# Kernel tuning notes

Measured on AMD Instinct MI355X. Metric: run time of the kernel, lower is better.

## Reference

```python
import jax, jax.numpy as jnp
import numpy as np

DIM = 1024

def setup_inputs() -> dict:
    key = jax.random.key(0)
    k1, k2, k3, k4 = jax.random.split(key, 4)
    scale = 1.0 / np.sqrt(DIM)
    return {
        "segment_embeds": jax.random.normal(k1, (32, 2048, DIM), dtype=jnp.float32),
        "Wq": jax.random.normal(k2, (DIM, DIM), dtype=jnp.float32) * scale,
        "bq": jax.random.normal(k3, (DIM,), dtype=jnp.float32) * scale,
        "mem_bank": jax.random.normal(k4, (131072, DIM), dtype=jnp.float32) * scale,
        "k": 8,
    }

def reference(segment_embeds, Wq, bq, mem_bank, k):
    # mean-pool over time: (B, C)
    segment_mean = segment_embeds.mean(axis=1)
    # linear query projection (torch Linear: x @ W.T + b)
    q = segment_mean @ Wq.T + bq
    # dense scores against memory bank: (B, M)
    attn_scores = (q @ mem_bank.T) / jnp.sqrt(jnp.asarray(DIM, dtype=q.dtype))
    # top-k select
    top_k_scores, top_k_indices = jax.lax.top_k(attn_scores, k)  # (B, K)
    attn_weights = jax.nn.softmax(top_k_scores, axis=-1)  # (B, K)
    # gather retrieved vectors: (B, K, C)
    retrieved_vectors = mem_bank[top_k_indices]
    # weighted sum over K, keepdim -> (B, 1, C)
    retrieved_mem = jnp.sum(attn_weights[..., None] * retrieved_vectors, axis=1, keepdims=True)
    return retrieved_mem
```

## Files before the change

kernel.cpp:

```cpp
#include <hip/hip_runtime.h>
#include <hip/hip_bf16.h>
#include <math.h>

#define NB 32
#define NT 2048
#define NC 1024
#define NM 131072
#define TOPK 8
#define PANELS 8
#define NSB 1024
#define SLOTF 260

typedef __attribute__((ext_vector_type(8))) short s16x8;
typedef __attribute__((ext_vector_type(4))) float f32x4;
typedef __attribute__((ext_vector_type(4))) int i32x4;

#define OFF_PART 0
#define OFF_CS   0
#define OFF_CI   262144
#define OFF_MEAN 1048576
#define OFF_Q    (OFF_MEAN + 32768)
#define OFF_QB   (OFF_Q + 32768)

__device__ __forceinline__ unsigned short f2bf(float f) {
    unsigned u = __float_as_uint(f);
    unsigned r = (u + 0x7FFFu + ((u >> 16) & 1u)) >> 16;
    return (unsigned short)r;
}

__device__ __forceinline__ void gl_lds16(const float* g, float* l) {
    __builtin_amdgcn_global_load_lds((const __attribute__((address_space(1))) void*)g,
                                     (__attribute__((address_space(3))) void*)l, 16, 0, 0);
}

__global__ __launch_bounds__(256) void mean_partial_k(const float* __restrict__ seg,
                                                      float* __restrict__ part) {
    int blk = blockIdx.x;
    int b = blk >> 5, tc = blk & 31;
    int tid = threadIdx.x;
    const float4* src = (const float4*)(seg + ((size_t)b * NT + (size_t)tc * 64) * NC);
    float4 acc = make_float4(0.f, 0.f, 0.f, 0.f);
#pragma unroll 4
    for (int t = 0; t < 64; ++t) {
        float4 v = src[(size_t)t * 256 + tid];
        acc.x += v.x; acc.y += v.y; acc.z += v.z; acc.w += v.w;
    }
    ((float4*)(part + ((size_t)b * 32 + tc) * NC))[tid] = acc;
}

__global__ __launch_bounds__(256) void mean_finalize_k(const float* __restrict__ part,
                                                       float* __restrict__ mean) {
    int i = blockIdx.x * 256 + threadIdx.x;
    int b = i >> 10, c = i & 1023;
    float s = 0.f;
#pragma unroll
    for (int tc = 0; tc < 32; ++tc) s += part[((size_t)b * 32 + tc) * NC + c];
    mean[i] = s * (1.0f / NT);
}

__global__ __launch_bounds__(256) void qproj_k(const float* __restrict__ mean,
                                               const float* __restrict__ Wq,
                                               const float* __restrict__ bq,
                                               float* __restrict__ q) {
    int wave = (blockIdx.x * 256 + threadIdx.x) >> 6;
    int lane = threadIdx.x & 63;
    int o0 = wave * 16;
    for (int j = 0; j < 16; ++j) {
        int o = o0 + j;
        int b = o >> 10, i = o & 1023;
        const float4* wr = (const float4*)(Wq + (size_t)i * NC);
        const float4* mr = (const float4*)(mean + (size_t)b * NC);
        float acc = 0.f;
#pragma unroll
        for (int e = 0; e < 4; ++e) {
            float4 w4 = wr[lane * 4 + e];
            float4 m4 = mr[lane * 4 + e];
            acc += w4.x * m4.x + w4.y * m4.y + w4.z * m4.z + w4.w * m4.w;
        }
#pragma unroll
        for (int off = 32; off; off >>= 1) acc += __shfl_xor(acc, off);
        if (lane == 0) q[o] = acc + bq[i];
    }
}

__global__ __launch_bounds__(256) void qbf_k(const float* __restrict__ q,
                                             s16x8* __restrict__ qb) {
    int idx = blockIdx.x * 256 + threadIdx.x;
    int lane = idx & 63, n = (idx >> 6) & 1, ks = idx >> 7;
    int b = n * 16 + (lane & 15);
    int k0 = ks * 32 + ((lane >> 4) << 3);
    s16x8 v;
#pragma unroll
    for (int e = 0; e < 8; ++e) v[e] = (short)f2bf(q[(size_t)b * NC + k0 + e]);
    qb[idx] = v;
}

#define BUBBLE8(v, vi, s, si)                                   \
    {                                                           \
        float _v = (v); int _vi = (vi);                         \
        _Pragma("unroll")                                       \
        for (int _u = 0; _u < 8; ++_u) {                        \
            bool _gt = _v > s[_u];                               \
            float _ts = _gt ? _v : s[_u];                       \
            int _ti = _gt ? _vi : si[_u];                       \
            _v = _gt ? s[_u] : _v;                              \
            _vi = _gt ? si[_u] : _vi;                           \
            s[_u] = _ts; si[_u] = _ti;                          \
        }                                                       \
    }

__global__ __launch_bounds__(64) void scores_mfma_k(const float* __restrict__ memb,
                                                    const s16x8* __restrict__ qb,
                                                    float* __restrict__ candS,
                                                    int* __restrict__ candI) {
    __shared__ __align__(16) float tiles[2 * 16 * SLOTF];
    __shared__ __align__(16) float sc[32 * 17];
    int lane = threadIdx.x;
    size_t mb0 = (size_t)blockIdx.x * (PANELS * 16);

    float s8[8]; int i8[8];
#pragma unroll
    for (int u = 0; u < 8; ++u) { s8[u] = -INFINITY; i8[u] = -1; }

#define TISSUE(t_) { int p_ = (t_) >> 2, c_ = (t_) & 3;                               \
    const float* rb_ = memb + (mb0 + p_ * 16) * NC + c_ * 256 + lane * 4;             \
    float* lb_ = tiles + ((t_) & 1) * (16 * SLOTF);                                   \
    _Pragma("unroll") for (int i_ = 0; i_ < 16; ++i_)                                 \
        gl_lds16(rb_ + (size_t)i_ * NC, lb_ + i_ * SLOTF); }

    f32x4 acc0 = (f32x4){0.f, 0.f, 0.f, 0.f};
    f32x4 acc1 = (f32x4){0.f, 0.f, 0.f, 0.f};

    TISSUE(0);
    for (int t = 0; t < PANELS * 4; ++t) {
        int c = t & 3;
        s16x8 qf[16];
#pragma unroll
        for (int k = 0; k < 8; ++k) {
            qf[2 * k]     = qb[((c * 8 + k) * 2 + 0) * 64 + lane];
            qf[2 * k + 1] = qb[((c * 8 + k) * 2 + 1) * 64 + lane];
        }
        asm volatile("s_waitcnt vmcnt(0)" ::: "memory");
        __builtin_amdgcn_sched_barrier(0);
        if (t + 1 < PANELS * 4) TISSUE(t + 1);

        const float* lanebase = tiles + (t & 1) * (16 * SLOTF)
                              + (lane & 15) * SLOTF + ((lane >> 4) << 3);
#pragma unroll
        for (int ks = 0; ks < 8; ++ks) {
            uint4 lo = *(const uint4*)(lanebase + ks * 32);
            uint4 hi = *(const uint4*)(lanebase + ks * 32 + 4);
            i32x4 ai;
            ai[0] = __builtin_amdgcn_perm(lo.y, lo.x, 0x07060302u);
            ai[1] = __builtin_amdgcn_perm(lo.w, lo.z, 0x07060302u);
            ai[2] = __builtin_amdgcn_perm(hi.y, hi.x, 0x07060302u);
            ai[3] = __builtin_amdgcn_perm(hi.w, hi.z, 0x07060302u);
            s16x8 a = __builtin_bit_cast(s16x8, ai);
            acc0 = __builtin_amdgcn_mfma_f32_16x16x32_bf16(a, qf[2 * ks], acc0, 0, 0, 0);
            acc1 = __builtin_amdgcn_mfma_f32_16x16x32_bf16(a, qf[2 * ks + 1], acc1, 0, 0, 0);
        }

        if (c == 3) {
            int p = t >> 2;
#pragma unroll
            for (int j = 0; j < 4; ++j) {
                sc[(0 * 16 + (lane & 15)) * 17 + ((lane >> 4) << 2) + j] = acc0[j];
                sc[(1 * 16 + (lane & 15)) * 17 + ((lane >> 4) << 2) + j] = acc1[j];
            }
            asm volatile("s_waitcnt lgkmcnt(0)" ::: "memory");
            __builtin_amdgcn_sched_barrier(0);
            int b = lane >> 1, p2 = lane & 1;
            int midx0 = mb0 + p * 16;
#pragma unroll
            for (int j = 0; j < 8; ++j) {
                int m = ((b + j) & 7) + p2 * 8;
                float v = sc[b * 17 + m];
                BUBBLE8(v, midx0 + m, s8, i8);
            }
            asm volatile("s_waitcnt lgkmcnt(0)" ::: "memory");
            __builtin_amdgcn_sched_barrier(0);
            acc0 = (f32x4){0.f, 0.f, 0.f, 0.f};
            acc1 = (f32x4){0.f, 0.f, 0.f, 0.f};
        }
    }
#undef TISSUE

    {
        float ov[8]; int oi[8];
#pragma unroll
        for (int u = 0; u < 8; ++u) { ov[u] = s8[u]; oi[u] = i8[u]; }
#pragma unroll
        for (int u = 0; u < 8; ++u) {
            float pv = __shfl_xor(ov[u], 1);
            int pi = __shfl_xor(oi[u], 1);
            BUBBLE8(pv, pi, s8, i8);
        }
        if ((lane & 1) == 0) {
            int b = lane >> 1;
#pragma unroll
            for (int u = 0; u < 8; ++u) {
                candS[(size_t)b * (NSB * 8) + blockIdx.x * 8 + u] = s8[u] * 0.03125f;
                candI[(size_t)b * (NSB * 8) + blockIdx.x * 8 + u] = i8[u];
            }
        }
    }
}

__global__ __launch_bounds__(256) void finalize_k(const float* __restrict__ candS,
                                                  const int* __restrict__ candI,
                                                  const float* __restrict__ memb,
                                                  const float* __restrict__ q,
                                                  float* __restrict__ out) {
    __shared__ float cs[256 * 9];
    __shared__ int ci[256 * 9];
    __shared__ float csA[64 * 9];
    __shared__ int ciA[64 * 9];
    __shared__ float exsc[64];
    __shared__ int exid[64];
    __shared__ float wgt[8];
    __shared__ int widx[8];
    int b = blockIdx.x, tid = threadIdx.x;
    const float* S = candS + (size_t)b * (NSB * 8);
    const int* I = candI + (size_t)b * (NSB * 8);

    {
        float s[8]; int si[8];
#pragma unroll
        for (int u = 0; u < 8; ++u) { s[u] = -INFINITY; si[u] = -1; }
        for (int j = 0; j < 32; ++j)
            BUBBLE8(S[tid * 32 + j], I[tid * 32 + j], s, si);
#pragma unroll
        for (int u = 0; u < 8; ++u) { cs[tid * 9 + u] = s[u]; ci[tid * 9 + u] = si[u]; }
    }
    __syncthreads();
    if (tid < 64) {
        float s[8]; int si[8];
#pragma unroll
        for (int u = 0; u < 8; ++u) { s[u] = -INFINITY; si[u] = -1; }
        for (int tt = 0; tt < 4; ++tt)
#pragma unroll
            for (int u = 0; u < 8; ++u)
                BUBBLE8(cs[(tid * 4 + tt) * 9 + u], ci[(tid * 4 + tt) * 9 + u], s, si);
#pragma unroll
        for (int u = 0; u < 8; ++u) { csA[tid * 9 + u] = s[u]; ciA[tid * 9 + u] = si[u]; }
    }
    __syncthreads();
    if (tid < 8) {
        float s[8]; int si[8];
#pragma unroll
        for (int u = 0; u < 8; ++u) { s[u] = -INFINITY; si[u] = -1; }
        for (int tt = 0; tt < 8; ++tt)
#pragma unroll
            for (int u = 0; u < 8; ++u)
                BUBBLE8(csA[(tid * 8 + tt) * 9 + u], ciA[(tid * 8 + tt) * 9 + u], s, si);
#pragma unroll
        for (int u = 0; u < 8; ++u) exid[tid * 8 + u] = si[u];
    }
    __syncthreads();
    {
        int w = tid >> 6, lane = tid & 63;
        const float4* qr = (const float4*)(q + (size_t)b * NC);
        for (int i = 0; i < 16; ++i) {
            int c = w * 16 + i;
            int row = exid[c];
            const float4* mr = (const float4*)(memb + (size_t)row * NC);
            float d = 0.f;
#pragma unroll
            for (int e = 0; e < 4; ++e) {
                float4 m4 = mr[e * 64 + lane];
                float4 q4 = qr[e * 64 + lane];
                d += m4.x * q4.x + m4.y * q4.y + m4.z * q4.z + m4.w * q4.w;
            }
#pragma unroll
            for (int off = 32; off; off >>= 1) d += __shfl_xor(d, off);
            if (lane == 0) exsc[c] = d * 0.03125f;
        }
    }
    __syncthreads();
    if (tid == 0) {
        float s4[8]; int si4[8];
#pragma unroll
        for (int u = 0; u < 8; ++u) { s4[u] = -INFINITY; si4[u] = -1; }
        for (int j = 0; j < 64; ++j)
            BUBBLE8(exsc[j], exid[j], s4, si4);
        float m = s4[0], sum = 0.f, w[8];
#pragma unroll
        for (int u = 0; u < 8; ++u) { w[u] = __expf(s4[u] - m); sum += w[u]; }
        float inv = 1.0f / sum;
#pragma unroll
        for (int u = 0; u < 8; ++u) { wgt[u] = w[u] * inv; widx[u] = si4[u]; }
    }
    __syncthreads();
    {
        float wv[8]; int ix[8];
#pragma unroll
        for (int u = 0; u < 8; ++u) { wv[u] = wgt[u]; ix[u] = widx[u]; }
        float4 o = make_float4(0.f, 0.f, 0.f, 0.f);
#pragma unroll
        for (int u = 0; u < 8; ++u) {
            float4 r = ((const float4*)(memb + (size_t)ix[u] * NC))[tid];
            o.x = fmaf(wv[u], r.x, o.x);
            o.y = fmaf(wv[u], r.y, o.y);
            o.z = fmaf(wv[u], r.z, o.z);
            o.w = fmaf(wv[u], r.w, o.w);
        }
        ((float4*)(out + (size_t)b * NC))[tid] = o;
    }
}

extern "C" void kernel_launch(void* const* d_in, const int* in_sizes, int n_in,
                              void* d_out, int out_size, void* d_ws, size_t ws_size,
                              hipStream_t stream) {
    const float* seg  = (const float*)d_in[0];
    const float* Wq   = (const float*)d_in[1];
    const float* bq   = (const float*)d_in[2];
    const float* memb = (const float*)d_in[3];
    float* ws = (float*)d_ws;
    float* part  = ws + OFF_PART;
    float* mean  = ws + OFF_MEAN;
    float* q     = ws + OFF_Q;
    s16x8* qb    = (s16x8*)(ws + OFF_QB);
    float* candS = ws + OFF_CS;
    int*   candI = (int*)(ws + OFF_CI);
    float* out = (float*)d_out;

    mean_partial_k<<<NB * 32, 256, 0, stream>>>(seg, part);
    mean_finalize_k<<<(NB * NC) / 256, 256, 0, stream>>>(part, mean);
    qproj_k<<<512, 256, 0, stream>>>(mean, Wq, bq, q);
    qbf_k<<<16, 256, 0, stream>>>(q, qb);
    scores_mfma_k<<<NSB, 64, 0, stream>>>(memb, qb, candS, candI);
    finalize_k<<<NB, 256, 0, stream>>>(candS, candI, memb, q, out);
}
```

Measured before the change: 213.6 us.

## Triple-buffer memory-bank tiles with deeper prefetch and double-buffered query fragments

```diff
diff --git a/kernel.cpp b/kernel.cpp
--- a/kernel.cpp
+++ b/kernel.cpp
@@ -7,8 +7,9 @@
 #define NC 1024
 #define NM 131072
 #define TOPK 8
-#define PANELS 8
-#define NSB 1024
+#define PANELS 16
+#define NSB 512
+#define NCHUNK (PANELS * 4)
 #define SLOTF 260
 
 typedef __attribute__((ext_vector_type(8))) short s16x8;
@@ -17,7 +18,7 @@
 
 #define OFF_PART 0
 #define OFF_CS   0
-#define OFF_CI   262144
+#define OFF_CI   131072
 #define OFF_MEAN 1048576
 #define OFF_Q    (OFF_MEAN + 32768)
 #define OFF_QB   (OFF_Q + 32768)
@@ -109,11 +110,11 @@
         }                                                       \
     }
 
-__global__ __launch_bounds__(64) void scores_mfma_k(const float* __restrict__ memb,
-                                                    const s16x8* __restrict__ qb,
-                                                    float* __restrict__ candS,
-                                                    int* __restrict__ candI) {
-    __shared__ __align__(16) float tiles[2 * 16 * SLOTF];
+__global__ __launch_bounds__(64, 1) void scores_mfma_k(const float* __restrict__ memb,
+                                                       const s16x8* __restrict__ qb,
+                                                       float* __restrict__ candS,
+                                                       int* __restrict__ candI) {
+    __shared__ __align__(16) float tiles[3 * 16 * SLOTF];
     __shared__ __align__(16) float sc[32 * 17];
     int lane = threadIdx.x;
     size_t mb0 = (size_t)blockIdx.x * (PANELS * 16);
@@ -124,66 +125,85 @@
 
 #define TISSUE(t_) { int p_ = (t_) >> 2, c_ = (t_) & 3;                               \
     const float* rb_ = memb + (mb0 + p_ * 16) * NC + c_ * 256 + lane * 4;             \
-    float* lb_ = tiles + ((t_) & 1) * (16 * SLOTF);                                   \
+    float* lb_ = tiles + ((t_) % 3) * (16 * SLOTF);                                   \
     _Pragma("unroll") for (int i_ = 0; i_ < 16; ++i_)                                 \
         gl_lds16(rb_ + (size_t)i_ * NC, lb_ + i_ * SLOTF); }
 
+#define QLOAD(dst_, t_) { int c_ = (t_) & 3;                                          \
+    _Pragma("unroll") for (int k_ = 0; k_ < 8; ++k_) {                                \
+        dst_[2 * k_]     = qb[((c_ * 8 + k_) * 2 + 0) * 64 + lane];                   \
+        dst_[2 * k_ + 1] = qb[((c_ * 8 + k_) * 2 + 1) * 64 + lane]; } }
+
+#define COMPUTE(t_, qf_) {                                                            \
+    const float* lanebase = tiles + ((t_) % 3) * (16 * SLOTF)                         \
+                          + (lane & 15) * SLOTF + ((lane >> 4) << 3);                 \
+    _Pragma("unroll") for (int ks = 0; ks < 8; ++ks) {                                \
+        uint4 lo = *(const uint4*)(lanebase + ks * 32);                               \
+        uint4 hi = *(const uint4*)(lanebase + ks * 32 + 4);                           \
+        i32x4 ai;                                                                     \
+        ai[0] = __builtin_amdgcn_perm(lo.y, lo.x, 0x07060302u);                       \
+        ai[1] = __builtin_amdgcn_perm(lo.w, lo.z, 0x07060302u);                       \
+        ai[2] = __builtin_amdgcn_perm(hi.y, hi.x, 0x07060302u);                       \
+        ai[3] = __builtin_amdgcn_perm(hi.w, hi.z, 0x07060302u);                       \
+        s16x8 a = __builtin_bit_cast(s16x8, ai);                                      \
+        acc0 = __builtin_amdgcn_mfma_f32_16x16x32_bf16(a, qf_[2 * ks], acc0, 0, 0, 0);\
+        acc1 = __builtin_amdgcn_mfma_f32_16x16x32_bf16(a, qf_[2 * ks + 1], acc1, 0, 0, 0); } \
+    if (((t_) & 3) == 3) {                                                            \
+        int p_ = (t_) >> 2;                                                           \
+        _Pragma("unroll") for (int j = 0; j < 4; ++j) {                               \
+            sc[(0 * 16 + (lane & 15)) * 17 + ((lane >> 4) << 2) + j] = acc0[j];       \
+            sc[(1 * 16 + (lane & 15)) * 17 + ((lane >> 4) << 2) + j] = acc1[j];       \
+        }                                                                             \
+        asm volatile("s_waitcnt lgkmcnt(0)" ::: "memory");                            \
+        __builtin_amdgcn_sched_barrier(0);                                            \
+        int b_ = lane >> 1, p2_ = lane & 1;                                           \
+        int midx0 = (int)mb0 + p_ * 16;                                               \
+        _Pragma("unroll") for (int j = 0; j < 8; ++j) {                               \
+            int m_ = ((b_ + j) & 7) + p2_ * 8;                                        \
+            float v_ = sc[b_ * 17 + m_];                                              \
+            BUBBLE8(v_, midx0 + m_, s8, i8);                                          \
+        }                                                                             \
+        asm volatile("s_waitcnt lgkmcnt(0)" ::: "memory");                            \
+        __builtin_amdgcn_sched_barrier(0);                                            \
+        acc0 = (f32x4){0.f, 0.f, 0.f, 0.f};                                           \
+        acc1 = (f32x4){0.f, 0.f, 0.f, 0.f};                                           \
+    } }
+
     f32x4 acc0 = (f32x4){0.f, 0.f, 0.f, 0.f};
     f32x4 acc1 = (f32x4){0.f, 0.f, 0.f, 0.f};
+    s16x8 qfA[16], qfB[16];
 
     TISSUE(0);
-    for (int t = 0; t < PANELS * 4; ++t) {
-        int c = t & 3;
-        s16x8 qf[16];
-#pragma unroll
-        for (int k = 0; k < 8; ++k) {
-            qf[2 * k]     = qb[((c * 8 + k) * 2 + 0) * 64 + lane];
-            qf[2 * k + 1] = qb[((c * 8 + k) * 2 + 1) * 64 + lane];
-        }
-        asm volatile("s_waitcnt vmcnt(0)" ::: "memory");
-        __builtin_amdgcn_sched_barrier(0);
-        if (t + 1 < PANELS * 4) TISSUE(t + 1);
-
-        const float* lanebase = tiles + (t & 1) * (16 * SLOTF)
-                              + (lane & 15) * SLOTF + ((lane >> 4) << 3);
-#pragma unroll
-        for (int ks = 0; ks < 8; ++ks) {
-            uint4 lo = *(const uint4*)(lanebase + ks * 32);
-            uint4 hi = *(const uint4*)(lanebase + ks * 32 + 4);
-            i32x4 ai;
-            ai[0] = __builtin_amdgcn_perm(lo.y, lo.x, 0x07060302u);
-            ai[1] = __builtin_amdgcn_perm(lo.w, lo.z, 0x07060302u);
-            ai[2] = __builtin_amdgcn_perm(hi.y, hi.x, 0x07060302u);
-            ai[3] = __builtin_amdgcn_perm(hi.w, hi.z, 0x07060302u);
-            s16x8 a = __builtin_bit_cast(s16x8, ai);
-            acc0 = __builtin_amdgcn_mfma_f32_16x16x32_bf16(a, qf[2 * ks], acc0, 0, 0, 0);
-            acc1 = __builtin_amdgcn_mfma_f32_16x16x32_bf16(a, qf[2 * ks + 1], acc1, 0, 0, 0);
-        }
-
-        if (c == 3) {
-            int p = t >> 2;
-#pragma unroll
-            for (int j = 0; j < 4; ++j) {
-                sc[(0 * 16 + (lane & 15)) * 17 + ((lane >> 4) << 2) + j] = acc0[j];
-                sc[(1 * 16 + (lane & 15)) * 17 + ((lane >> 4) << 2) + j] = acc1[j];
-            }
-            asm volatile("s_waitcnt lgkmcnt(0)" ::: "memory");
-            __builtin_amdgcn_sched_barrier(0);
-            int b = lane >> 1, p2 = lane & 1;
-            int midx0 = mb0 + p * 16;
-#pragma unroll
-            for (int j = 0; j < 8; ++j) {
-                int m = ((b + j) & 7) + p2 * 8;
-                float v = sc[b * 17 + m];
-                BUBBLE8(v, midx0 + m, s8, i8);
-            }
-            asm volatile("s_waitcnt lgkmcnt(0)" ::: "memory");
-            __builtin_amdgcn_sched_barrier(0);
-            acc0 = (f32x4){0.f, 0.f, 0.f, 0.f};
-            acc1 = (f32x4){0.f, 0.f, 0.f, 0.f};
-        }
+    __builtin_amdgcn_sched_barrier(0);
+    QLOAD(qfA, 0);
+    __builtin_amdgcn_sched_barrier(0);
+    TISSUE(1);
+    __builtin_amdgcn_sched_barrier(0);
+
+    for (int t = 0; t < NCHUNK; t += 2) {
+        asm volatile("s_waitcnt vmcnt(16)" ::: "memory");
+        __builtin_amdgcn_sched_barrier(0);
+        QLOAD(qfB, t + 1);
+        __builtin_amdgcn_sched_barrier(0);
+        if (t + 2 < NCHUNK) TISSUE(t + 2);
+        __builtin_amdgcn_sched_barrier(0);
+        COMPUTE(t, qfA);
+
+        if (t + 2 < NCHUNK) {
+            asm volatile("s_waitcnt vmcnt(16)" ::: "memory");
+        } else {
+            asm volatile("s_waitcnt vmcnt(0)" ::: "memory");
+        }
+        __builtin_amdgcn_sched_barrier(0);
+        if (t + 2 < NCHUNK) QLOAD(qfA, t + 2);
+        __builtin_amdgcn_sched_barrier(0);
+        if (t + 3 < NCHUNK) TISSUE(t + 3);
+        __builtin_amdgcn_sched_barrier(0);
+        COMPUTE(t + 1, qfB);
     }
 #undef TISSUE
+#undef QLOAD
+#undef COMPUTE
 
     {
         float ov[8]; int oi[8];
@@ -227,8 +247,8 @@
         float s[8]; int si[8];
 #pragma unroll
         for (int u = 0; u < 8; ++u) { s[u] = -INFINITY; si[u] = -1; }
-        for (int j = 0; j < 32; ++j)
-            BUBBLE8(S[tid * 32 + j], I[tid * 32 + j], s, si);
+        for (int j = 0; j < 16; ++j)
+            BUBBLE8(S[tid * 16 + j], I[tid * 16 + j], s, si);
 #pragma unroll
         for (int u = 0; u < 8; ++u) { cs[tid * 9 + u] = s[u]; ci[tid * 9 + u] = si[u]; }
     }
```

New measurement: 208.9 us. 1.02x faster.
